# Kernel optimization log

Hardware: AMD Instinct MI355X
Metric: run time of the kernel (lower is better)

The kernel has to match this reference:

```python
import jax, jax.numpy as jnp
import numpy as np

N = 50000        # nodes
E = 800000       # edges (before self-loops)
IN = 512         # in_channels
HEADS = 8        # 'head' arg: heads and per-head out dim of conv1
C1 = 8           # per-head channels of conv1 (== head)
OUT = 128        # out_channels of conv2
NEG_SLOPE = 0.2  # PyG GATConv leaky-relu slope


def _glorot(key, shape, fan_in):
    return jax.random.normal(key, shape, jnp.float32) * (1.0 / np.sqrt(fan_in))


def setup_inputs() -> dict:
    key = jax.random.key(0)
    ks = jax.random.split(key, 10)
    x = jax.random.normal(ks[0], (N, IN), jnp.float32)
    edge_index = jax.random.randint(ks[1], (2, E), 0, N, dtype=jnp.int32)
    # conv1: GATConv(IN, C1, heads=HEADS, concat=True)
    W1 = _glorot(ks[2], (IN, HEADS * C1), IN)
    att_src1 = _glorot(ks[3], (HEADS, C1), C1)
    att_dst1 = _glorot(ks[4], (HEADS, C1), C1)
    bias1 = jnp.zeros((HEADS * C1,), jnp.float32)
    # conv2: GATConv(HEADS*C1, OUT, heads=1, concat=False)
    W2 = _glorot(ks[5], (HEADS * C1, OUT), HEADS * C1)
    att_src2 = _glorot(ks[6], (1, OUT), OUT)
    att_dst2 = _glorot(ks[7], (1, OUT), OUT)
    bias2 = jnp.zeros((OUT,), jnp.float32)
    return {"x": x, "edge_index": edge_index,
            "W1": W1, "att_src1": att_src1, "att_dst1": att_dst1, "bias1": bias1,
            "W2": W2, "att_src2": att_src2, "att_dst2": att_dst2, "bias2": bias2}


def gat_conv(x, src, dst, W, a_src, a_dst, bias, heads, concat):
    """PyG GATConv (eval mode, dropout off). src/dst already include self-loops."""
    n = x.shape[0]
    h = (x @ W).reshape(n, heads, -1)                 # [N, H, C]
    s = (h * a_src[None]).sum(-1)                     # [N, H] alpha_src per node
    d = (h * a_dst[None]).sum(-1)                     # [N, H] alpha_dst per node
    alpha = jax.nn.leaky_relu(s[src] + d[dst], NEG_SLOPE)  # [E, H]
    # segment softmax over incoming edges of each destination node
    amax = jax.ops.segment_max(alpha, dst, num_segments=n)  # [N, H]
    amax = jnp.where(jnp.isfinite(amax), amax, 0.0)
    ea = jnp.exp(alpha - amax[dst])                   # [E, H]
    denom = jax.ops.segment_sum(ea, dst, num_segments=n)
    w = ea / (denom[dst] + 1e-16)                     # [E, H]
    msg = h[src] * w[..., None]                       # [E, H, C]
    out = jax.ops.segment_sum(msg, dst, num_segments=n)  # [N, H, C]
    out = out.reshape(n, -1) if concat else out.mean(axis=1)
    return out + bias


def reference(x, edge_index, W1, att_src1, att_dst1, bias1,
              W2, att_src2, att_dst2, bias2):
    n = x.shape[0]
    loop = jnp.arange(n, dtype=edge_index.dtype)      # PyG adds self-loops
    src = jnp.concatenate([edge_index[0], loop])
    dst = jnp.concatenate([edge_index[1], loop])
    h = jax.nn.elu(gat_conv(x, src, dst, W1, att_src1, att_dst1, bias1,
                            heads=HEADS, concat=True))
    out = jax.nn.elu(gat_conv(h, src, dst, W2, att_src2, att_dst2, bias2,
                              heads=1, concat=False))
    return out
```

## Files before the change

### kernel.cpp

```cpp
#include <hip/hip_runtime.h>

#define NEG_SLOPE 0.2f
#define CAP 128

typedef __attribute__((ext_vector_type(8))) short bf16x8;
typedef __attribute__((ext_vector_type(4))) float f32x4;

__device__ __forceinline__ float leaky(float v) {
    return v > 0.0f ? v : NEG_SLOPE * v;
}
__device__ __forceinline__ float elu(float v) {
    return v > 0.0f ? v : (__expf(v) - 1.0f);
}
__device__ __forceinline__ short f2b(float f) {
    return (short)((__float_as_uint(f) + 0x8000u) >> 16);
}
__device__ __forceinline__ float bf2f(unsigned short v) {
    return __uint_as_float(((unsigned)v) << 16);
}

__global__ void prep_k(const float* __restrict__ W1, const float* __restrict__ W2,
                       unsigned short* __restrict__ w1s, unsigned short* __restrict__ w2s,
                       int* __restrict__ wp, int N) {
    int i = blockIdx.x * 256 + threadIdx.x;
    if (i < N) wp[i] = 0;
    if (i < 512 * 64) {
        int k = i >> 6, n = i & 63;
        int kt = k >> 5, kk = k & 31;
        int nt = n >> 4, nn = n & 15;
        int lane = (kk >> 3) * 16 + nn, j = kk & 7;
        w1s[(((size_t)(kt * 4 + nt)) * 64 + lane) * 8 + j] = (unsigned short)f2b(W1[i]);
    } else if (i < 512 * 64 + 64 * 128) {
        int i2 = i - 512 * 64;
        int k = i2 >> 7, n = i2 & 127;
        int kt = k >> 5, kk = k & 31;
        int nt = n >> 4, nn = n & 15;
        int lane = (kk >> 3) * 16 + nn, j = kk & 7;
        w2s[(((size_t)(kt * 8 + nt)) * 64 + lane) * 8 + j] = (unsigned short)f2b(W2[i2]);
    }
}

__global__ __launch_bounds__(256) void gemm1_k(const float* __restrict__ X,
                                               const unsigned short* __restrict__ Ws,
                                               const float* __restrict__ Asrc,
                                               const float* __restrict__ Adst,
                                               unsigned short* __restrict__ Hb,
                                               float* __restrict__ S,
                                               float* __restrict__ D, int N) {
    const int lane = threadIdx.x & 63;
    const int wave = threadIdx.x >> 6;
    const int m0 = blockIdx.x * 64 + wave * 16;
    const int q = lane >> 4, lc = lane & 15;
    const int arow = m0 + lc;
    const float* xrow = X + (size_t)min(arow, N - 1) * 512 + q * 8;
    const bf16x8* bW = (const bf16x8*)Ws;

    f32x4 acc[4] = {{0.f,0.f,0.f,0.f},{0.f,0.f,0.f,0.f},{0.f,0.f,0.f,0.f},{0.f,0.f,0.f,0.f}};

    for (int g = 0; g < 2; ++g) {
        float4 a[16];
#pragma unroll
        for (int u = 0; u < 16; ++u)
            a[u] = *(const float4*)(xrow + g * 256 + (u >> 1) * 32 + (u & 1) * 4);
#pragma unroll
        for (int u2 = 0; u2 < 8; ++u2) {
            const int kt = g * 8 + u2;
            float4 a0 = a[u2 * 2], a1 = a[u2 * 2 + 1];
            bf16x8 af;
            af[0] = f2b(a0.x); af[1] = f2b(a0.y); af[2] = f2b(a0.z); af[3] = f2b(a0.w);
            af[4] = f2b(a1.x); af[5] = f2b(a1.y); af[6] = f2b(a1.z); af[7] = f2b(a1.w);
#pragma unroll
            for (int nt = 0; nt < 4; ++nt) {
                bf16x8 bf = bW[(size_t)(kt * 4 + nt) * 64 + lane];
                acc[nt] = __builtin_amdgcn_mfma_f32_16x16x32_bf16(af, bf, acc[nt], 0, 0, 0);
            }
        }
    }

    float asc[4], adc[4];
#pragma unroll
    for (int nt = 0; nt < 4; ++nt) { asc[nt] = Asrc[nt * 16 + lc]; adc[nt] = Adst[nt * 16 + lc]; }

#pragma unroll
    for (int r = 0; r < 4; ++r) {
        int row = m0 + q * 4 + r;
        bool ok = row < N;
        if (ok) {
#pragma unroll
            for (int nt = 0; nt < 4; ++nt)
                Hb[(size_t)row * 64 + nt * 16 + lc] = (unsigned short)f2b(acc[nt][r]);
        }
        float ps[4], pd[4];
#pragma unroll
        for (int nt = 0; nt < 4; ++nt) { ps[nt] = acc[nt][r] * asc[nt]; pd[nt] = acc[nt][r] * adc[nt]; }
#pragma unroll
        for (int off = 1; off < 8; off <<= 1) {
#pragma unroll
            for (int nt = 0; nt < 4; ++nt) {
                ps[nt] += __shfl_xor(ps[nt], off);
                pd[nt] += __shfl_xor(pd[nt], off);
            }
        }
        if (ok && !(lc & 7)) {
            int hb = lc >> 3;
#pragma unroll
            for (int nt = 0; nt < 4; ++nt) {
                S[(size_t)row * 8 + nt * 2 + hb] = ps[nt];
                D[(size_t)row * 8 + nt * 2 + hb] = pd[nt];
            }
        }
    }
}

__global__ __launch_bounds__(256) void pack_k(const int* __restrict__ ei, int E,
                                              int* __restrict__ wp, int* __restrict__ srcs) {
    int e = blockIdx.x * 256 + threadIdx.x;
    if (e < E) {
        int s = ei[e];
        int d = ei[E + e];
        int c = atomicAdd(&wp[d], 1);
        if (c < CAP) srcs[((size_t)d << 7) + c] = s;
    }
}

__global__ __launch_bounds__(256) void agg1g2_k(const int* __restrict__ wp,
                                                const int* __restrict__ srcs,
                                                const float* __restrict__ S1,
                                                const float* __restrict__ D1,
                                                const unsigned short* __restrict__ H1b,
                                                const float* __restrict__ b1,
                                                const unsigned short* __restrict__ W2s,
                                                const float* __restrict__ as2,
                                                const float* __restrict__ ad2,
                                                unsigned short* __restrict__ H2b,
                                                float* __restrict__ S2,
                                                float* __restrict__ D2, int N) {
    __shared__ unsigned short sh[16][64];
    __shared__ float shp[4][16], shq[4][16];

    const int tid  = threadIdx.x;
    const int lane = tid & 63;
    const int wave = tid >> 6;
    const int m0 = blockIdx.x * 16;

    const int h = lane & 7;
    const int eg = lane >> 3;
#pragma unroll
    for (int rep = 0; rep < 4; ++rep) {
        const int nl = wave * 4 + rep;
        const int wid = m0 + nl;
        if (wid < N) {
            const int deg = min(wp[wid], CAP);
            const size_t b0 = (size_t)wid << 7;
            const float dvh = D1[(size_t)wid * 8 + h];

            float wself = __expf(leaky(S1[(size_t)wid * 8 + h] + dvh));
            float den = (eg == 0) ? wself : 0.0f;
            float acc[8] = {0.f,0.f,0.f,0.f,0.f,0.f,0.f,0.f};
            if (eg == 0) {
                bf16x8 hv = *(const bf16x8*)(H1b + (size_t)wid * 64 + h * 8);
#pragma unroll
                for (int c = 0; c < 8; ++c)
                    acc[c] = wself * bf2f((unsigned short)hv[c]);
            }

            for (int base = 0; base < deg; base += 8) {
                int i = base + eg;
                bool v = i < deg;
                int src = v ? srcs[b0 + i] : wid;
                float w = v ? __expf(leaky(S1[(size_t)src * 8 + h] + dvh)) : 0.0f;
                den += w;
                bf16x8 hv = *(const bf16x8*)(H1b + (size_t)src * 64 + h * 8);
#pragma unroll
                for (int c = 0; c < 8; ++c)
                    acc[c] += w * bf2f((unsigned short)hv[c]);
            }
#pragma unroll
            for (int off = 8; off < 64; off <<= 1) {
                den += __shfl_xor(den, off);
#pragma unroll
                for (int c = 0; c < 8; ++c)
                    acc[c] += __shfl_xor(acc[c], off);
            }
            if (eg == 0) {
                const float rden = 1.0f / (den + 1e-16f);
                bf16x8 o;
#pragma unroll
                for (int c = 0; c < 8; ++c)
                    o[c] = f2b(elu(acc[c] * rden + b1[h * 8 + c]));
                *(bf16x8*)(&sh[nl][h * 8]) = o;
            }
        } else if (eg == 0) {
            *(bf16x8*)(&sh[nl][h * 8]) = bf16x8{0,0,0,0,0,0,0,0};
        }
    }
    __syncthreads();

    const int q = lane >> 4, lc = lane & 15;
    const bf16x8* bW = (const bf16x8*)W2s;
    const int nt0 = wave * 2;

    f32x4 acc2[2] = {{0.f,0.f,0.f,0.f},{0.f,0.f,0.f,0.f}};
#pragma unroll
    for (int kt = 0; kt < 2; ++kt) {
        bf16x8 af = *(const bf16x8*)(&sh[lc][q * 8 + kt * 32]);
#pragma unroll
        for (int u = 0; u < 2; ++u) {
            bf16x8 bf = bW[(size_t)(kt * 8 + nt0 + u) * 64 + lane];
            acc2[u] = __builtin_amdgcn_mfma_f32_16x16x32_bf16(af, bf, acc2[u], 0, 0, 0);
        }
    }
    float asc[2], adc[2];
#pragma unroll
    for (int u = 0; u < 2; ++u) {
        asc[u] = as2[(nt0 + u) * 16 + lc];
        adc[u] = ad2[(nt0 + u) * 16 + lc];
    }
#pragma unroll
    for (int r = 0; r < 4; ++r) {
        int rl = q * 4 + r;
        int row = m0 + rl;
        if (row < N) {
#pragma unroll
            for (int u = 0; u < 2; ++u)
                H2b[(size_t)row * 128 + (nt0 + u) * 16 + lc] = (unsigned short)f2b(acc2[u][r]);
        }
        float ps = acc2[0][r] * asc[0] + acc2[1][r] * asc[1];
        float pd = acc2[0][r] * adc[0] + acc2[1][r] * adc[1];
#pragma unroll
        for (int off = 1; off < 16; off <<= 1) {
            ps += __shfl_xor(ps, off);
            pd += __shfl_xor(pd, off);
        }
        if (lc == 0) { shp[wave][rl] = ps; shq[wave][rl] = pd; }
    }
    __syncthreads();
    if (tid < 16) {
        int row = m0 + tid;
        if (row < N) {
            float s = shp[0][tid] + shp[1][tid] + shp[2][tid] + shp[3][tid];
            float d = shq[0][tid] + shq[1][tid] + shq[2][tid] + shq[3][tid];
            S2[row] = s;
            D2[row] = d;
        }
    }
}

__global__ __launch_bounds__(256) void agg2_k(const int* __restrict__ wp,
                                              const int* __restrict__ srcs,
                                              const float* __restrict__ S,
                                              const float* __restrict__ D,
                                              const unsigned short* __restrict__ Hb,
                                              const float* __restrict__ bias,
                                              float* __restrict__ out, int N) {
    const int wid = (blockIdx.x * 256 + threadIdx.x) >> 6;
    const int lane = threadIdx.x & 63;
    if (wid >= N) return;
    const int deg = min(wp[wid], CAP);
    const size_t b0 = (size_t)wid << 7;
    const float dv = D[wid];
    const int eg = lane >> 3;
    const int sl = lane & 7;
    const int c0 = sl * 16;

    const float wself = __expf(leaky(S[wid] + dv));
    float den = (eg == 0) ? wself : 0.0f;
    float acc[16] = {0.f,0.f,0.f,0.f,0.f,0.f,0.f,0.f,
                     0.f,0.f,0.f,0.f,0.f,0.f,0.f,0.f};
    if (eg == 0) {
        bf16x8 hv0 = *(const bf16x8*)(Hb + (size_t)wid * 128 + c0);
        bf16x8 hv1 = *(const bf16x8*)(Hb + (size_t)wid * 128 + c0 + 8);
#pragma unroll
        for (int c = 0; c < 8; ++c) {
            acc[c]     = wself * bf2f((unsigned short)hv0[c]);
            acc[c + 8] = wself * bf2f((unsigned short)hv1[c]);
        }
    }

    for (int base = 0; base < deg; base += 8) {
        int i = base + eg;
        bool v = i < deg;
        int src = v ? srcs[b0 + i] : wid;
        float w = v ? __expf(leaky(S[src] + dv)) : 0.0f;
        den += w;
        bf16x8 hv0 = *(const bf16x8*)(Hb + (size_t)src * 128 + c0);
        bf16x8 hv1 = *(const bf16x8*)(Hb + (size_t)src * 128 + c0 + 8);
#pragma unroll
        for (int c = 0; c < 8; ++c) {
            acc[c]     += w * bf2f((unsigned short)hv0[c]);
            acc[c + 8] += w * bf2f((unsigned short)hv1[c]);
        }
    }
#pragma unroll
    for (int off = 1; off < 64; off <<= 1)
        den += __shfl_xor(den, off);
#pragma unroll
    for (int off = 8; off < 64; off <<= 1) {
#pragma unroll
        for (int c = 0; c < 16; ++c)
            acc[c] += __shfl_xor(acc[c], off);
    }
    if (eg == 0) {
        const float rden = 1.0f / (den * 0.125f + 1e-16f);
        float4 o[4];
#pragma unroll
        for (int u = 0; u < 4; ++u) {
            o[u].x = elu(acc[u * 4 + 0] * rden + bias[c0 + u * 4 + 0]);
            o[u].y = elu(acc[u * 4 + 1] * rden + bias[c0 + u * 4 + 1]);
            o[u].z = elu(acc[u * 4 + 2] * rden + bias[c0 + u * 4 + 2]);
            o[u].w = elu(acc[u * 4 + 3] * rden + bias[c0 + u * 4 + 3]);
        }
#pragma unroll
        for (int u = 0; u < 4; ++u)
            *(float4*)(out + (size_t)wid * 128 + c0 + u * 4) = o[u];
    }
}

extern "C" void kernel_launch(void* const* d_in, const int* in_sizes, int n_in,
                              void* d_out, int out_size, void* d_ws, size_t ws_size,
                              hipStream_t stream) {
    const float* x   = (const float*)d_in[0];
    const int*   ei  = (const int*)d_in[1];
    const float* W1  = (const float*)d_in[2];
    const float* as1 = (const float*)d_in[3];
    const float* ad1 = (const float*)d_in[4];
    const float* b1  = (const float*)d_in[5];
    const float* W2  = (const float*)d_in[6];
    const float* as2 = (const float*)d_in[7];
    const float* ad2 = (const float*)d_in[8];
    const float* b2  = (const float*)d_in[9];

    const int N = in_sizes[0] / 512;
    const int E = in_sizes[1] / 2;

    unsigned short* w1s  = (unsigned short*)d_ws;
    unsigned short* w2s  = w1s + 512 * 64;
    unsigned short* h1b  = w2s + 64 * 128;
    unsigned short* h2b  = h1b + (size_t)N * 64;
    float*          s1   = (float*)(h2b + (size_t)N * 128);
    float*          d1   = s1 + (size_t)N * 8;
    float*          s2   = d1 + (size_t)N * 8;
    float*          d2   = s2 + N;
    int*            wp   = (int*)(d2 + N);
    int*            srcs = wp + N;

    const int B = 256;
    const int gblk = (N + 63) / 64;
    int prep_n = 512 * 64 + 64 * 128;
    if (N > prep_n) prep_n = N;

    prep_k<<<(prep_n + B - 1) / B, B, 0, stream>>>(W1, W2, w1s, w2s, wp, N);
    gemm1_k<<<gblk, B, 0, stream>>>(x, w1s, as1, ad1, h1b, s1, d1, N);
    pack_k<<<(E + B - 1) / B, B, 0, stream>>>(ei, E, wp, srcs);
    agg1g2_k<<<(N + 15) / 16, B, 0, stream>>>(wp, srcs, s1, d1, h1b, b1,
                                              w2s, as2, ad2, h2b, s2, d2, N);
    agg2_k<<<(N + 3) / 4, B, 0, stream>>>(wp, srcs, s2, d2, h2b, b2,
                                          (float*)d_out, N);
}
```

Before: 327.6 us.

## Stage X tiles into LDS via global_load_lds with XOR swizzle in gemm1

Replaces the per-lane strided float4 global loads of X in the first GEMM with coalesced 16-byte direct-to-LDS loads of 64x128 float tiles, using an XOR swizzle to avoid bank conflicts on the read side. The goal is better global coalescing for the 512-wide fp32 input, which dominates this bandwidth-bound GEMM. It adds two barriers per K-chunk and 32KB of LDS per block, which may reduce occupancy, and the loads are not double-buffered.

```diff
diff --git a/kernel.cpp b/kernel.cpp
--- a/kernel.cpp
+++ b/kernel.cpp
@@ -47,25 +47,43 @@
                                                unsigned short* __restrict__ Hb,
                                                float* __restrict__ S,
                                                float* __restrict__ D, int N) {
-    const int lane = threadIdx.x & 63;
-    const int wave = threadIdx.x >> 6;
-    const int m0 = blockIdx.x * 64 + wave * 16;
+    __shared__ float xs[64 * 128];
+    const int tid  = threadIdx.x;
+    const int lane = tid & 63;
+    const int wave = tid >> 6;
+    const int bm0  = blockIdx.x * 64;
+    const int m0   = bm0 + wave * 16;
     const int q = lane >> 4, lc = lane & 15;
-    const int arow = m0 + lc;
-    const float* xrow = X + (size_t)min(arow, N - 1) * 512 + q * 8;
     const bf16x8* bW = (const bf16x8*)Ws;
 
     f32x4 acc[4] = {{0.f,0.f,0.f,0.f},{0.f,0.f,0.f,0.f},{0.f,0.f,0.f,0.f},{0.f,0.f,0.f,0.f}};
 
-    for (int g = 0; g < 2; ++g) {
-        float4 a[16];
-#pragma unroll
-        for (int u = 0; u < 16; ++u)
-            a[u] = *(const float4*)(xrow + g * 256 + (u >> 1) * 32 + (u & 1) * 4);
-#pragma unroll
-        for (int u2 = 0; u2 < 8; ++u2) {
-            const int kt = g * 8 + u2;
-            float4 a0 = a[u2 * 2], a1 = a[u2 * 2 + 1];
+    auto* lds3 = (__attribute__((address_space(3))) char*)xs;
+
+    for (int g = 0; g < 4; ++g) {
+        __syncthreads();
+#pragma unroll
+        for (int p = 0; p < 8; ++p) {
+            const int L   = p * 256 + tid;
+            const int row = L >> 5;
+            const int cs  = ((L & 31) ^ (row & 7)) << 2;
+            const int grow = min(bm0 + row, N - 1);
+            const float* src = X + (size_t)grow * 512 + g * 128 + cs;
+            __builtin_amdgcn_global_load_lds(
+                (const __attribute__((address_space(1))) unsigned int*)src,
+                (__attribute__((address_space(3))) unsigned int*)
+                    (lds3 + (size_t)(p * 256 + wave * 64) * 16),
+                16, 0, 0);
+        }
+        __syncthreads();
+#pragma unroll
+        for (int ktl = 0; ktl < 4; ++ktl) {
+            const int kt  = g * 4 + ktl;
+            const int row = wave * 16 + lc;
+            const int c   = q * 8 + ktl * 32;
+            const int r7  = row & 7;
+            const float4 a0 = *(const float4*)&xs[row * 128 + (((c >> 2) ^ r7) << 2)];
+            const float4 a1 = *(const float4*)&xs[row * 128 + ((((c >> 2) + 1) ^ r7) << 2)];
             bf16x8 af;
             af[0] = f2b(a0.x); af[1] = f2b(a0.y); af[2] = f2b(a0.z); af[3] = f2b(a0.w);
             af[4] = f2b(a1.x); af[5] = f2b(a1.y); af[6] = f2b(a1.z); af[7] = f2b(a1.w);
```

Result: no change. 330.1 us (+0.8%).
